# Performance work log

Measured on AMD Instinct MI355X. Metric: run time of the kernel, lower is better.

The kernel has to match this reference:

```python
import jax, jax.numpy as jnp
import numpy as np

L, D_MODEL, D_INNER, DT_RANK, D_STATE, D_CONV, VOCAB = 4, 768, 1536, 48, 16, 4, 32000
B, S = 1, 1024


def rmsnorm(x, w, eps=1e-5):
    return x * jax.lax.rsqrt(jnp.mean(x * x, axis=-1, keepdims=True) + eps) * w


def causal_depthwise_conv(x, w, b):
    # x: [B,S,D]; w: [D,1,K] (torch Conv1d groups=D weight layout); causal left-pad K-1
    y = jax.lax.conv_general_dilated(
        x.transpose(0, 2, 1), w, window_strides=(1,), padding=[(D_CONV - 1, 0)],
        dimension_numbers=('NCH', 'OIH', 'NCH'), feature_group_count=D_INNER)
    return y.transpose(0, 2, 1) + b


def selective_scan(u, dt, A, Bm, Cm, Dv):
    # Faithful to the source: A_delta = exp(dt (x) A), clamp(min=-20) is a no-op on exp output
    A_delta = jnp.clip(jnp.exp(jnp.einsum('bld,dn->bldn', dt, A)), -20.0, None)
    B_delta_u = jnp.einsum('bld,bld,bln->bldn', dt, u, Bm)
    shifted = jnp.pad(A_delta[:, 1:], ((0, 0), (1, 0), (0, 0), (0, 0)))
    A_cum = jnp.exp(jnp.cumsum(shifted, axis=1))
    h = B_delta_u / (A_cum + 1e-12)
    y = jnp.einsum('bldn,bln->bld', jnp.cumsum(h, axis=1) * A_cum, Cm)
    return y + u * Dv


def setup_inputs() -> dict:
    key = jax.random.key(0)
    ks = jax.random.split(key, 8)
    return {
        'tokens': jax.random.randint(ks[0], (B, S), 0, VOCAB),
        'embedding': jax.random.normal(ks[1], (VOCAB, D_MODEL), jnp.float32) * 0.02,
        'norm_w': jnp.ones((L, D_MODEL), jnp.float32),
        'in_proj_w': jax.random.normal(ks[2], (L, 2 * D_INNER, D_MODEL), jnp.float32) * 0.02,
        'conv_w': jax.random.normal(ks[3], (L, D_INNER, 1, D_CONV), jnp.float32) * 0.2,
        'conv_b': jnp.zeros((L, D_INNER), jnp.float32),
        'x_proj_w': jax.random.normal(ks[4], (L, DT_RANK + 2 * D_STATE, D_INNER), jnp.float32) * 0.02,
        'dt_proj_w': jax.random.normal(ks[5], (L, D_INNER, DT_RANK), jnp.float32) * 0.001,
        'dt_proj_b': jnp.full((L, D_INNER), 5.0, jnp.float32),  # delta~5 keeps exp(cumsum(exp(dt*A))) finite
        'A_log': jnp.tile(jnp.log(jnp.arange(1, D_STATE + 1, dtype=jnp.float32)), (L, D_INNER, 1)),
        'D_skip': jnp.ones((L, D_INNER), jnp.float32),
        'out_proj_w': jax.random.normal(ks[6], (L, D_MODEL, D_INNER), jnp.float32) * 0.02,
        'final_norm_w': jnp.ones((D_MODEL,), jnp.float32),
    }


def reference(tokens, embedding, norm_w, in_proj_w, conv_w, conv_b, x_proj_w,
              dt_proj_w, dt_proj_b, A_log, D_skip, out_proj_w, final_norm_w):
    x = embedding[tokens]  # [B,S,d_model]
    for i in range(L):
        h = rmsnorm(x, norm_w[i])
        xz = h @ in_proj_w[i].T                      # [B,S,2*d_inner]
        xi, res = xz[..., :D_INNER], xz[..., D_INNER:]
        xi = jax.nn.silu(causal_depthwise_conv(xi, conv_w[i], conv_b[i]))
        proj = xi @ x_proj_w[i].T                    # [B,S,dt_rank+2*d_state]
        dt = jax.nn.softplus(proj[..., :DT_RANK] @ dt_proj_w[i].T + dt_proj_b[i])
        Bm = proj[..., DT_RANK:DT_RANK + D_STATE]
        Cm = proj[..., DT_RANK + D_STATE:]
        A = -jnp.exp(A_log[i])                       # [d_inner, d_state]
        y = selective_scan(xi, dt, A, Bm, Cm, D_skip[i])
        x = x + (y * jax.nn.silu(res)) @ out_proj_w[i].T
    return rmsnorm(x, final_norm_w) @ embedding.T    # tied LM head: [B,S,vocab]
```

## Files before the change

### kernel.cpp

```cpp
#include <hip/hip_runtime.h>
#include <hip/hip_bf16.h>
#include <cmath>

namespace {

constexpr int kL      = 4;
constexpr int kDModel = 768;
constexpr int kDInner = 1536;
constexpr int kDtRank = 48;
constexpr int kDState = 16;
constexpr int kDConv  = 4;
constexpr int kSeq    = 1024;
constexpr int kPLd    = 96;
constexpr int kPB     = 128;
constexpr int kVocab  = 32000;
constexpr int kCH     = 64;
constexpr int kNCH    = kSeq / kCH;
constexpr int kDN     = kDInner * kDState;

using short8 = __attribute__((ext_vector_type(8))) short;
using f32x4  = __attribute__((ext_vector_type(4))) float;

__device__ __forceinline__ float silu_f(float v) {
    return v / (1.f + __expf(-v));
}

__device__ __forceinline__ void split_bf16(float v, __hip_bfloat16& hi, __hip_bfloat16& lo) {
    hi = __float2bfloat16(v);
    lo = __float2bfloat16(v - __bfloat162float(hi));
}

__global__ void __launch_bounds__(256) f2b_kernel(
    const float* __restrict__ src, __hip_bfloat16* __restrict__ dst, int n) {
    int i = (blockIdx.x * 256 + threadIdx.x) * 4;
    const int stride = gridDim.x * 256 * 4;
    for (; i + 3 < n; i += stride) {
        const float4 v = *reinterpret_cast<const float4*>(src + i);
        dst[i + 0] = __float2bfloat16(v.x);
        dst[i + 1] = __float2bfloat16(v.y);
        dst[i + 2] = __float2bfloat16(v.z);
        dst[i + 3] = __float2bfloat16(v.w);
    }
}

__global__ void __launch_bounds__(256) split3_kernel(
    const float* __restrict__ src, int ldsrc, int rows, int cols,
    __hip_bfloat16* __restrict__ dst, int rowsPad) {
    const int idx = blockIdx.x * 256 + threadIdx.x;
    if (idx >= rowsPad * cols) return;
    const int r = idx / cols, c = idx % cols;
    const float v = (r < rows) ? src[(size_t)r * ldsrc + c] : 0.f;
    __hip_bfloat16 hi, lo;
    split_bf16(v, hi, lo);
    __hip_bfloat16* row = dst + (size_t)r * 3 * cols;
    row[c] = hi; row[cols + c] = hi; row[2 * cols + c] = lo;
}

__global__ void __launch_bounds__(256) dup2_kernel(
    const float* __restrict__ src, __hip_bfloat16* __restrict__ dst, int rows, int cols) {
    const int idx = blockIdx.x * 256 + threadIdx.x;
    if (idx >= rows * cols) return;
    const int r = idx / cols, c = idx % cols;
    const __hip_bfloat16 hi = __float2bfloat16(src[(size_t)r * cols + c]);
    __hip_bfloat16* row = dst + (size_t)r * 2 * cols;
    row[c] = hi; row[cols + c] = hi;
}

__global__ void __launch_bounds__(256) split3x_kernel(
    const float* __restrict__ src, __hip_bfloat16* __restrict__ dst) {
    const int idx = blockIdx.x * 256 + threadIdx.x;
    if (idx >= kL * kPB * kDInner) return;
    const int layer = idx / (kPB * kDInner);
    const int rem   = idx % (kPB * kDInner);
    const int r = rem / kDInner, c = rem % kDInner;
    const float v = (r < kDtRank + 2 * kDState)
        ? src[(size_t)layer * (kDtRank + 2 * kDState) * kDInner + (size_t)r * kDInner + c]
        : 0.f;
    __hip_bfloat16 hi, lo;
    split_bf16(v, hi, lo);
    __hip_bfloat16* row = dst + ((size_t)layer * kPB + r) * 3 * kDInner;
    row[c] = hi; row[kDInner + c] = hi; row[2 * kDInner + c] = lo;
}

__global__ void __launch_bounds__(256) embed_rms_kernel(
    const int* __restrict__ tokens, const float* __restrict__ emb,
    const float* __restrict__ w, float* __restrict__ x,
    __hip_bfloat16* __restrict__ h2) {
    const int s = blockIdx.x;
    const int t = tokens[s];
    const float* src = emb + (size_t)t * kDModel;
    float v[3];
    float ss = 0.f;
    #pragma unroll
    for (int j = 0; j < 3; ++j) {
        const int d = threadIdx.x + j * 256;
        v[j] = src[d];
        x[(size_t)s * kDModel + d] = v[j];
        ss = fmaf(v[j], v[j], ss);
    }
    #pragma unroll
    for (int m = 32; m; m >>= 1) ss += __shfl_xor(ss, m);
    __shared__ float red[4];
    if ((threadIdx.x & 63) == 0) red[threadIdx.x >> 6] = ss;
    __syncthreads();
    const float total = red[0] + red[1] + red[2] + red[3];
    const float scale = rsqrtf(total / (float)kDModel + 1e-5f);
    __hip_bfloat16* dst = h2 + (size_t)s * 3 * kDModel;
    #pragma unroll
    for (int j = 0; j < 3; ++j) {
        const int d = threadIdx.x + j * 256;
        const float hv = v[j] * scale * w[d];
        __hip_bfloat16 hi, lo;
        split_bf16(hv, hi, lo);
        dst[d] = hi; dst[kDModel + d] = lo; dst[2 * kDModel + d] = hi;
    }
}

template <bool FINAL>
__global__ void __launch_bounds__(256) reduce_rms_kernel(
    const float* __restrict__ parts, size_t stride,
    const float* __restrict__ w, float* __restrict__ x,
    __hip_bfloat16* __restrict__ out) {
    const int s = blockIdx.x;
    float v[3];
    float ss = 0.f;
    #pragma unroll
    for (int j = 0; j < 3; ++j) {
        const int d = threadIdx.x + j * 256;
        const size_t off = (size_t)s * kDModel + d;
        float acc = x[off];
        #pragma unroll
        for (int p = 0; p < 6; ++p) acc += parts[(size_t)p * stride + off];
        v[j] = acc;
        x[off] = acc;
        ss = fmaf(acc, acc, ss);
    }
    #pragma unroll
    for (int m = 32; m; m >>= 1) ss += __shfl_xor(ss, m);
    __shared__ float red[4];
    if ((threadIdx.x & 63) == 0) red[threadIdx.x >> 6] = ss;
    __syncthreads();
    const float total = red[0] + red[1] + red[2] + red[3];
    const float scale = rsqrtf(total / (float)kDModel + 1e-5f);
    #pragma unroll
    for (int j = 0; j < 3; ++j) {
        const int d = threadIdx.x + j * 256;
        const float hv = v[j] * scale * w[d];
        if (FINAL) {
            out[(size_t)s * kDModel + d] = __float2bfloat16(hv);
        } else {
            __hip_bfloat16 hi, lo;
            split_bf16(hv, hi, lo);
            __hip_bfloat16* dst = out + (size_t)s * 3 * kDModel;
            dst[d] = hi; dst[kDModel + d] = lo; dst[2 * kDModel + d] = hi;
        }
    }
}

template <int BM, int BN, int KSPLIT>
__global__ void __launch_bounds__(256) mfma_gemm(
    const __hip_bfloat16* __restrict__ A, int lda,
    const __hip_bfloat16* __restrict__ B, int ldb,
    float* __restrict__ C, int ldc,
    int N, int K, size_t partStride) {
    constexpr int BK = 32;
    static_assert(BM == 128 && BN == 128, "staging assumes 128x128");
    __shared__ unsigned short As[2][BM * BK];
    __shared__ unsigned short Bs[2][BN * BK];
    const int tid  = threadIdx.x;
    const int lane = tid & 63;

    const int nwg = gridDim.x * gridDim.y;
    int bid = blockIdx.y * gridDim.x + blockIdx.x;
    {
        const int q = nwg >> 3, r = nwg & 7;
        const int xcd = bid & 7, pos = bid >> 3;
        bid = (xcd < r ? xcd * (q + 1) : r * (q + 1) + (xcd - r) * q) + pos;
    }
    const int m0 = (bid % gridDim.x) * BM;
    const int n0 = (bid / gridDim.x) * BN;

    const int Kp = K / KSPLIT;
    const int kbeg = (KSPLIT > 1) ? blockIdx.z * Kp : 0;
    float* Cw = (KSPLIT > 1) ? C + (size_t)blockIdx.z * partStride : C;
    constexpr int WM = BM / 2, WN = BN / 2;
    constexpr int MR = WM / 16, NR = WN / 16;
    const int wave = tid >> 6;
    const int wm = (wave >> 1) * WM, wn = (wave & 1) * WN;
    const int l15 = lane & 15, l4 = lane >> 4;
    f32x4 acc[MR][NR] = {};

    auto stage = [&](int buf, int k0) {
        #pragma unroll
        for (int i = 0; i < 2; ++i) {
            const int idx = tid + i * 256;
            const int r = idx >> 2, qv = idx & 3;
            const int qs = qv ^ ((r >> 1) & 3);
            __builtin_amdgcn_global_load_lds(
                (const __attribute__((address_space(1))) void*)(A + (size_t)(m0 + r) * lda + k0 + qs * 8),
                (__attribute__((address_space(3))) void*)(&As[buf][(idx - lane) * 8]),
                16, 0, 0);
        }
        #pragma unroll
        for (int i = 0; i < 2; ++i) {
            const int idx = tid + i * 256;
            const int r = idx >> 2, qv = idx & 3;
            const int qs = qv ^ ((r >> 1) & 3);
            __builtin_amdgcn_global_load_lds(
                (const __attribute__((address_space(1))) void*)(B + (size_t)(n0 + r) * ldb + k0 + qs * 8),
                (__attribute__((address_space(3))) void*)(&Bs[buf][(idx - lane) * 8]),
                16, 0, 0);
        }
    };

    const int nt = Kp / BK;
    int cur = 0;
    stage(0, kbeg);
    for (int t = 0; t < nt; ++t) {
        if (t + 1 < nt) {
            stage(cur ^ 1, kbeg + (t + 1) * BK);
            asm volatile("s_waitcnt vmcnt(4)" ::: "memory");
        } else {
            asm volatile("s_waitcnt vmcnt(0)" ::: "memory");
        }
        __builtin_amdgcn_s_barrier();

        short8 af[MR], bfv[NR];
        #pragma unroll
        for (int mi = 0; mi < MR; ++mi) {
            const int R = wm + mi * 16 + l15;
            af[mi] = *reinterpret_cast<const short8*>(&As[cur][(R * 4 + (l4 ^ ((R >> 1) & 3))) * 8]);
        }
        #pragma unroll
        for (int ni = 0; ni < NR; ++ni) {
            const int R = wn + ni * 16 + l15;
            bfv[ni] = *reinterpret_cast<const short8*>(&Bs[cur][(R * 4 + (l4 ^ ((R >> 1) & 3))) * 8]);
        }
        #pragma unroll
        for (int mi = 0; mi < MR; ++mi)
            #pragma unroll
            for (int ni = 0; ni < NR; ++ni)
                acc[mi][ni] = __builtin_amdgcn_mfma_f32_16x16x32_bf16(
                    af[mi], bfv[ni], acc[mi][ni], 0, 0, 0);

        asm volatile("s_waitcnt lgkmcnt(0)" ::: "memory");
        __builtin_amdgcn_s_barrier();
        cur ^= 1;
    }

    #pragma unroll
    for (int mi = 0; mi < MR; ++mi) {
        const int mrow = m0 + wm + mi * 16 + l4 * 4;
        #pragma unroll
        for (int ni = 0; ni < NR; ++ni) {
            const int ncol = n0 + wn + ni * 16 + l15;
            if (ncol >= N) continue;
            #pragma unroll
            for (int r = 0; r < 4; ++r)
                Cw[(size_t)(mrow + r) * ldc + ncol] = acc[mi][ni][r];
        }
    }
}

template <int NP>
__global__ void __launch_bounds__(256) reduce_parts(
    const float* __restrict__ parts, size_t stride,
    float* __restrict__ dst, int count) {
    const int i = (blockIdx.x * 256 + threadIdx.x) * 4;
    if (i >= count) return;
    float4 s = *reinterpret_cast<const float4*>(parts + i);
    #pragma unroll
    for (int p = 1; p < NP; ++p) {
        const float4 v = *reinterpret_cast<const float4*>(parts + (size_t)p * stride + i);
        s.x += v.x; s.y += v.y; s.z += v.z; s.w += v.w;
    }
    *reinterpret_cast<float4*>(dst + i) = s;
}

__global__ void __launch_bounds__(256) conv_silu_kernel(
    const float* __restrict__ p0, const float* __restrict__ p1,
    const float* __restrict__ cw, const float* __restrict__ cb,
    float* __restrict__ xi, __hip_bfloat16* __restrict__ xi2) {
    const int s = blockIdx.x;
    const int d = blockIdx.y * 256 + threadIdx.x;
    float acc = cb[d];
    #pragma unroll
    for (int k = 0; k < kDConv; ++k) {
        const int sl = s - (kDConv - 1) + k;
        if (sl >= 0) {
            const size_t off = (size_t)sl * (2 * kDInner) + d;
            acc = fmaf(p0[off] + p1[off], cw[d * kDConv + k], acc);
        }
    }
    const float v = silu_f(acc);
    xi[(size_t)s * kDInner + d] = v;
    __hip_bfloat16 hi, lo;
    split_bf16(v, hi, lo);
    __hip_bfloat16* row = xi2 + (size_t)s * 3 * kDInner;
    row[d] = hi; row[kDInner + d] = lo; row[2 * kDInner + d] = hi;
}


__device__ __forceinline__ void compute_dt_tile(
    const float* __restrict__ proj, const float* __restrict__ dtw,
    const float* __restrict__ dtb, int l0, int d0, int tid,
    float (*sP)[kDtRank], float (*sdtw)[kDtRank + 1], float (*sdt)[16]) {
    for (int idx = tid; idx < kCH * kDtRank; idx += 256) {
        const int r = idx / kDtRank, c = idx % kDtRank;
        sP[r][c] = proj[(size_t)(l0 + r) * kPLd + c];
    }
    for (int idx = tid; idx < 16 * kDtRank; idx += 256) {
        const int dd = idx / kDtRank, c = idx % kDtRank;
        sdtw[dd][c] = dtw[(size_t)(d0 + dd) * kDtRank + c];
    }
    __syncthreads();
    #pragma unroll
    for (int e = 0; e < 4; ++e) {
        const int idx = tid + e * 256;
        const int r = idx >> 4, dd = idx & 15;
        float acc = dtb[d0 + dd];
        #pragma unroll
        for (int k = 0; k < kDtRank; ++k)
            acc = fmaf(sP[r][k], sdtw[dd][k], acc);
        acc = (acc > 20.f) ? acc : log1pf(__expf(acc));
        sdt[r][dd] = acc;
    }
}

__global__ void __launch_bounds__(256) scan_part1(
    const float* __restrict__ u, const float* __restrict__ proj,
    const float* __restrict__ A_log, const float* __restrict__ dtw,
    const float* __restrict__ dtb,
    float* __restrict__ P, float* __restrict__ S) {
    __shared__ float sP[kCH][kDtRank];
    __shared__ float sdtw[16][kDtRank + 1];
    __shared__ float sdt[kCH][16], su[kCH][16], sB[kCH][16];
    const int tid = threadIdx.x;
    const int n = tid & 15, dl = tid >> 4;
    const int d0 = blockIdx.x * 16;
    const int l0 = blockIdx.y * kCH;
    for (int idx = tid; idx < kCH * 16; idx += 256) {
        const int r = idx >> 4, c = idx & 15;
        su[r][c] = u[(size_t)(l0 + r) * kDInner + d0 + c];
        sB[r][c] = proj[(size_t)(l0 + r) * kPLd + kDtRank + c];
    }
    compute_dt_tile(proj, dtw, dtb, l0, d0, tid, sP, sdtw, sdt);
    __syncthreads();
    const int d = d0 + dl;
    const float Adn = -__expf(A_log[d * kDState + n]);
    float state = 0.f, sumA = 0.f;
    #pragma unroll 8
    for (int l = 0; l < kCH; ++l) {
        const float dtv = sdt[l][dl];
        const float adelta = __expf(dtv * Adn);
        const float mult = __expf(adelta);
        state = fmaf(state, mult, dtv * su[l][dl] * sB[l][n]);
        sumA += adelta;
    }
    const int dn = d * kDState + n;
    P[(size_t)blockIdx.y * kDN + dn] = __expf(sumA);
    S[(size_t)blockIdx.y * kDN + dn] = state;
}

__global__ void __launch_bounds__(256) scan_part2(
    const float* __restrict__ u, const float* __restrict__ proj,
    const float* __restrict__ A_log, const float* __restrict__ dtw,
    const float* __restrict__ dtb, const float* __restrict__ D_skip,
    const float* __restrict__ P, const float* __restrict__ S,
    const float* __restrict__ res0, const float* __restrict__ res1,
    __hip_bfloat16* __restrict__ g2) {
    __shared__ float sP[kCH][kDtRank];
    __shared__ float sdtw[16][kDtRank + 1];
    __shared__ float sdt[kCH][16], su[kCH][16], sB[kCH][16], sC[kCH][16];
    __shared__ float sy[kCH][16];
    const int tid = threadIdx.x;
    const int n = tid & 15, dl = tid >> 4;
    const int d0 = blockIdx.x * 16;
    const int l0 = blockIdx.y * kCH;
    for (int idx = tid; idx < kCH * 16; idx += 256) {
        const int r = idx >> 4, c = idx & 15;
        su[r][c] = u[(size_t)(l0 + r) * kDInner + d0 + c];
        sB[r][c] = proj[(size_t)(l0 + r) * kPLd + kDtRank + c];
        sC[r][c] = proj[(size_t)(l0 + r) * kPLd + kDtRank + kDState + c];
    }
    compute_dt_tile(proj, dtw, dtb, l0, d0, tid, sP, sdtw, sdt);
    const int dn = d0 * kDState + tid;
    float state = 0.f;
    for (int jj = 0; jj < (int)blockIdx.y; ++jj) {
        const size_t idx = (size_t)jj * kDN + dn;
        state = fmaf(state, P[idx], S[idx]);
    }
    __syncthreads();
    const int d = d0 + dl;
    const float Adn = -__expf(A_log[d * kDState + n]);
    const float Dv  = D_skip[d];
    for (int l = 0; l < kCH; ++l) {
        const float dtv = sdt[l][dl];
        const float uv  = su[l][dl];
        const float mult = __expf(__expf(dtv * Adn));
        state = fmaf(state, mult, dtv * uv * sB[l][n]);
        float contrib = state * sC[l][n];
        contrib += __shfl_xor(contrib, 8);
        contrib += __shfl_xor(contrib, 4);
        contrib += __shfl_xor(contrib, 2);
        contrib += __shfl_xor(contrib, 1);
        if (n == 0) sy[l][dl] = fmaf(uv, Dv, contrib);
    }
    __syncthreads();
    for (int idx = tid; idx < kCH * 16; idx += 256) {
        const int r = idx >> 4, c = idx & 15;
        const size_t roff = (size_t)(l0 + r) * (2 * kDInner) + kDInner + d0 + c;
        const float res = res0[roff] + res1[roff];
        const float v = sy[r][c] * silu_f(res);
        __hip_bfloat16 hi, lo;
        split_bf16(v, hi, lo);
        __hip_bfloat16* row = g2 + (size_t)(l0 + r) * 2 * kDInner;
        row[d0 + c] = hi; row[kDInner + d0 + c] = lo;
    }
}

}

extern "C" void kernel_launch(void* const* d_in, const int* in_sizes, int n_in,
                              void* d_out, int out_size, void* d_ws, size_t ws_size,
                              hipStream_t stream) {
    const int*   tokens       = (const int*)d_in[0];
    const float* embedding    = (const float*)d_in[1];
    const float* norm_w       = (const float*)d_in[2];
    const float* in_proj_w    = (const float*)d_in[3];
    const float* conv_w       = (const float*)d_in[4];
    const float* conv_b       = (const float*)d_in[5];
    const float* x_proj_w     = (const float*)d_in[6];
    const float* dt_proj_w    = (const float*)d_in[7];
    const float* dt_proj_b    = (const float*)d_in[8];
    const float* A_log        = (const float*)d_in[9];
    const float* D_skip       = (const float*)d_in[10];
    const float* out_proj_w   = (const float*)d_in[11];
    const float* final_norm_w = (const float*)d_in[12];
    float* out = (float*)d_out;

    constexpr int K3m = 3 * kDModel;
    constexpr int K3i = 3 * kDInner;
    constexpr int K2i = 2 * kDInner;

    char* ws = (char*)d_ws;
    auto alloc = [&](size_t bytes) { char* p = ws; ws += (bytes + 255) & ~(size_t)255; return p; };
    float* x    = (float*)alloc((size_t)kSeq * kDModel * 4);
    float* xi   = (float*)alloc((size_t)kSeq * kDInner * 4);
    float* proj = (float*)alloc((size_t)kSeq * kPLd * 4);
    float* scanP  = (float*)alloc((size_t)kNCH * kDN * 4);
    float* scanS  = (float*)alloc((size_t)kNCH * kDN * 4);
    float* partsXZ = (float*)alloc((size_t)2 * kSeq * 2 * kDInner * 4);
    float* partsP  = (float*)alloc((size_t)24 * kSeq * kPLd * 4);
    float* partsO  = (float*)alloc((size_t)6 * kSeq * kDModel * 4);
    __hip_bfloat16* h_bf   = (__hip_bfloat16*)alloc((size_t)kSeq * kDModel * 2);
    __hip_bfloat16* h2     = (__hip_bfloat16*)alloc((size_t)kSeq * K3m * 2);
    __hip_bfloat16* xi2    = (__hip_bfloat16*)alloc((size_t)kSeq * K3i * 2);
    __hip_bfloat16* g2     = (__hip_bfloat16*)alloc((size_t)kSeq * K2i * 2);
    __hip_bfloat16* emb_bf = (__hip_bfloat16*)alloc((size_t)kVocab * kDModel * 2);
    __hip_bfloat16* inw2   = (__hip_bfloat16*)alloc((size_t)kL * 2 * kDInner * K3m * 2);
    __hip_bfloat16* outw2  = (__hip_bfloat16*)alloc((size_t)kL * kDModel * K2i * 2);
    __hip_bfloat16* xw2    = (__hip_bfloat16*)alloc((size_t)kL * kPB * K3i * 2);

    f2b_kernel<<<4096, 256, 0, stream>>>(embedding, emb_bf, kVocab * kDModel);
    dup2_kernel<<<(kL * kDModel * kDInner + 255) / 256, 256, 0, stream>>>(
        out_proj_w, outw2, kL * kDModel, kDInner);
    split3_kernel<<<(kL * 2 * kDInner * kDModel + 255) / 256, 256, 0, stream>>>(
        in_proj_w, kDModel, kL * 2 * kDInner, kDModel, inw2, kL * 2 * kDInner);
    split3x_kernel<<<(kL * kPB * kDInner + 255) / 256, 256, 0, stream>>>(
        x_proj_w, xw2);

    embed_rms_kernel<<<kSeq, 256, 0, stream>>>(tokens, embedding, norm_w, x, h2);

    for (int i = 0; i < kL; ++i) {
        mfma_gemm<128, 128, 2><<<dim3(kSeq / 128, 2 * kDInner / 128, 2), 256, 0, stream>>>(
            h2, K3m, inw2 + (size_t)i * 2 * kDInner * K3m, K3m,
            partsXZ, 2 * kDInner, 2 * kDInner, K3m, (size_t)kSeq * 2 * kDInner);

        conv_silu_kernel<<<dim3(kSeq, kDInner / 256), 256, 0, stream>>>(
            partsXZ, partsXZ + (size_t)kSeq * 2 * kDInner,
            conv_w + (size_t)i * kDInner * kDConv, conv_b + (size_t)i * kDInner,
            xi, xi2);

        mfma_gemm<128, 128, 24><<<dim3(kSeq / 128, 1, 24), 256, 0, stream>>>(
            xi2, K3i, xw2 + (size_t)i * kPB * K3i, K3i,
            partsP, kPLd, kPLd, K3i, (size_t)kSeq * kPLd);
        reduce_parts<24><<<(kSeq * kPLd / 4 + 255) / 256, 256, 0, stream>>>(
            partsP, (size_t)kSeq * kPLd, proj, kSeq * kPLd);

        const float* A_l  = A_log + (size_t)i * kDInner * kDState;
        const float* dtw  = dt_proj_w + (size_t)i * kDInner * kDtRank;
        const float* dtb  = dt_proj_b + (size_t)i * kDInner;
        scan_part1<<<dim3(kDInner / 16, kNCH), 256, 0, stream>>>(
            xi, proj, A_l, dtw, dtb, scanP, scanS);
        scan_part2<<<dim3(kDInner / 16, kNCH), 256, 0, stream>>>(
            xi, proj, A_l, dtw, dtb, D_skip + (size_t)i * kDInner,
            scanP, scanS, partsXZ, partsXZ + (size_t)kSeq * 2 * kDInner, g2);

        mfma_gemm<128, 128, 6><<<dim3(kSeq / 128, kDModel / 128, 6), 256, 0, stream>>>(
            g2, K2i, outw2 + (size_t)i * kDModel * K2i, K2i,
            partsO, kDModel, kDModel, K2i, (size_t)kSeq * kDModel);

        if (i + 1 < kL) {
            reduce_rms_kernel<false><<<kSeq, 256, 0, stream>>>(
                partsO, (size_t)kSeq * kDModel, norm_w + (size_t)(i + 1) * kDModel, x, h2);
        } else {
            reduce_rms_kernel<true><<<kSeq, 256, 0, stream>>>(
                partsO, (size_t)kSeq * kDModel, final_norm_w, x, h_bf);
        }
    }

    mfma_gemm<128, 128, 1><<<dim3(kSeq / 128, kVocab / 128, 1), 256, 0, stream>>>(
        h_bf, kDModel, emb_bf, kDModel, out, kVocab, kVocab, kDModel, 0);
}
```

Baseline: 777.6 us.

## Vectorize weight conversion kernels and raise split-K factors for in/out projections

The f32-to-bf16 weight conversion and duplication kernels now process four or eight elements per thread with vector loads and packed stores, instead of scalar element-wise writes. Split-K for the in_proj GEMM rises from 2 to 4 and for out_proj from 6 to 8, giving more blocks per launch. The consumers (conv_silu, scan_part2, reduce_rms) now sum a variable number of partial buffers. In exchange, the larger split writes and reads more fp32 partial data per layer.

```diff
diff --git a/kernel.cpp b/kernel.cpp
--- a/kernel.cpp
+++ b/kernel.cpp
@@ -17,12 +17,19 @@
 constexpr int kCH     = 64;
 constexpr int kNCH    = kSeq / kCH;
 constexpr int kDN     = kDInner * kDState;
+constexpr int kSplitIn  = 4;
+constexpr int kSplitOut = 8;
 
 using short8 = __attribute__((ext_vector_type(8))) short;
 using f32x4  = __attribute__((ext_vector_type(4))) float;
 
 __device__ __forceinline__ float silu_f(float v) {
     return v / (1.f + __expf(-v));
+}
+
+__device__ __forceinline__ unsigned short f2bu(float v) {
+    __hip_bfloat16 h = __float2bfloat16(v);
+    return *reinterpret_cast<unsigned short*>(&h);
 }
 
 __device__ __forceinline__ void split_bf16(float v, __hip_bfloat16& hi, __hip_bfloat16& lo) {
@@ -30,56 +37,78 @@
     lo = __float2bfloat16(v - __bfloat162float(hi));
 }
 
+__device__ __forceinline__ void split_u(float v, unsigned short& hi, unsigned short& lo) {
+    __hip_bfloat16 h, l;
+    split_bf16(v, h, l);
+    hi = *reinterpret_cast<unsigned short*>(&h);
+    lo = *reinterpret_cast<unsigned short*>(&l);
+}
+
 __global__ void __launch_bounds__(256) f2b_kernel(
     const float* __restrict__ src, __hip_bfloat16* __restrict__ dst, int n) {
-    int i = (blockIdx.x * 256 + threadIdx.x) * 4;
-    const int stride = gridDim.x * 256 * 4;
-    for (; i + 3 < n; i += stride) {
-        const float4 v = *reinterpret_cast<const float4*>(src + i);
-        dst[i + 0] = __float2bfloat16(v.x);
-        dst[i + 1] = __float2bfloat16(v.y);
-        dst[i + 2] = __float2bfloat16(v.z);
-        dst[i + 3] = __float2bfloat16(v.w);
+    int i = (blockIdx.x * 256 + threadIdx.x) * 8;
+    const int stride = gridDim.x * 256 * 8;
+    for (; i + 7 < n; i += stride) {
+        const float4 a = *reinterpret_cast<const float4*>(src + i);
+        const float4 b = *reinterpret_cast<const float4*>(src + i + 4);
+        union { unsigned short u[8]; uint4 v; } pk;
+        pk.u[0] = f2bu(a.x); pk.u[1] = f2bu(a.y); pk.u[2] = f2bu(a.z); pk.u[3] = f2bu(a.w);
+        pk.u[4] = f2bu(b.x); pk.u[5] = f2bu(b.y); pk.u[6] = f2bu(b.z); pk.u[7] = f2bu(b.w);
+        *reinterpret_cast<uint4*>(reinterpret_cast<unsigned short*>(dst) + i) = pk.v;
     }
 }
 
 __global__ void __launch_bounds__(256) split3_kernel(
-    const float* __restrict__ src, int ldsrc, int rows, int cols,
-    __hip_bfloat16* __restrict__ dst, int rowsPad) {
+    const float* __restrict__ src, int rows, int cols,
+    __hip_bfloat16* __restrict__ dst) {
     const int idx = blockIdx.x * 256 + threadIdx.x;
-    if (idx >= rowsPad * cols) return;
-    const int r = idx / cols, c = idx % cols;
-    const float v = (r < rows) ? src[(size_t)r * ldsrc + c] : 0.f;
-    __hip_bfloat16 hi, lo;
-    split_bf16(v, hi, lo);
-    __hip_bfloat16* row = dst + (size_t)r * 3 * cols;
-    row[c] = hi; row[cols + c] = hi; row[2 * cols + c] = lo;
+    const int c4cnt = cols >> 2;
+    if (idx >= rows * c4cnt) return;
+    const int r = idx / c4cnt, c = (idx % c4cnt) << 2;
+    const float4 v = *reinterpret_cast<const float4*>(src + (size_t)r * cols + c);
+    ushort4 hi4, lo4;
+    split_u(v.x, hi4.x, lo4.x); split_u(v.y, hi4.y, lo4.y);
+    split_u(v.z, hi4.z, lo4.z); split_u(v.w, hi4.w, lo4.w);
+    unsigned short* row = reinterpret_cast<unsigned short*>(dst) + (size_t)r * 3 * cols;
+    *reinterpret_cast<ushort4*>(row + c) = hi4;
+    *reinterpret_cast<ushort4*>(row + cols + c) = hi4;
+    *reinterpret_cast<ushort4*>(row + 2 * cols + c) = lo4;
 }
 
 __global__ void __launch_bounds__(256) dup2_kernel(
-    const float* __restrict__ src, __hip_bfloat16* __restrict__ dst, int rows, int cols) {
+    const float* __restrict__ src, __hip_bfloat16* __restrict__ dst,
+    int rows, int cols) {
     const int idx = blockIdx.x * 256 + threadIdx.x;
-    if (idx >= rows * cols) return;
-    const int r = idx / cols, c = idx % cols;
-    const __hip_bfloat16 hi = __float2bfloat16(src[(size_t)r * cols + c]);
-    __hip_bfloat16* row = dst + (size_t)r * 2 * cols;
-    row[c] = hi; row[cols + c] = hi;
+    const int c4cnt = cols >> 2;
+    if (idx >= rows * c4cnt) return;
+    const int r = idx / c4cnt, c = (idx % c4cnt) << 2;
+    const float4 v = *reinterpret_cast<const float4*>(src + (size_t)r * cols + c);
+    ushort4 hi4 = {f2bu(v.x), f2bu(v.y), f2bu(v.z), f2bu(v.w)};
+    unsigned short* row = reinterpret_cast<unsigned short*>(dst) + (size_t)r * 2 * cols;
+    *reinterpret_cast<ushort4*>(row + c) = hi4;
+    *reinterpret_cast<ushort4*>(row + cols + c) = hi4;
 }
 
 __global__ void __launch_bounds__(256) split3x_kernel(
     const float* __restrict__ src, __hip_bfloat16* __restrict__ dst) {
     const int idx = blockIdx.x * 256 + threadIdx.x;
-    if (idx >= kL * kPB * kDInner) return;
-    const int layer = idx / (kPB * kDInner);
-    const int rem   = idx % (kPB * kDInner);
-    const int r = rem / kDInner, c = rem % kDInner;
-    const float v = (r < kDtRank + 2 * kDState)
-        ? src[(size_t)layer * (kDtRank + 2 * kDState) * kDInner + (size_t)r * kDInner + c]
-        : 0.f;
-    __hip_bfloat16 hi, lo;
-    split_bf16(v, hi, lo);
-    __hip_bfloat16* row = dst + ((size_t)layer * kPB + r) * 3 * kDInner;
-    row[c] = hi; row[kDInner + c] = hi; row[2 * kDInner + c] = lo;
+    constexpr int c4cnt = kDInner >> 2;
+    if (idx >= kL * kPB * c4cnt) return;
+    const int layer = idx / (kPB * c4cnt);
+    const int rem   = idx % (kPB * c4cnt);
+    const int r = rem / c4cnt, c = (rem % c4cnt) << 2;
+    float4 v = {0.f, 0.f, 0.f, 0.f};
+    if (r < kDtRank + 2 * kDState)
+        v = *reinterpret_cast<const float4*>(
+            src + (size_t)layer * (kDtRank + 2 * kDState) * kDInner + (size_t)r * kDInner + c);
+    ushort4 hi4, lo4;
+    split_u(v.x, hi4.x, lo4.x); split_u(v.y, hi4.y, lo4.y);
+    split_u(v.z, hi4.z, lo4.z); split_u(v.w, hi4.w, lo4.w);
+    unsigned short* row = reinterpret_cast<unsigned short*>(dst)
+        + ((size_t)layer * kPB + r) * 3 * kDInner;
+    *reinterpret_cast<ushort4*>(row + c) = hi4;
+    *reinterpret_cast<ushort4*>(row + kDInner + c) = hi4;
+    *reinterpret_cast<ushort4*>(row + 2 * kDInner + c) = lo4;
 }
 
 __global__ void __launch_bounds__(256) embed_rms_kernel(
@@ -130,7 +159,7 @@
         const size_t off = (size_t)s * kDModel + d;
         float acc = x[off];
         #pragma unroll
-        for (int p = 0; p < 6; ++p) acc += parts[(size_t)p * stride + off];
+        for (int p = 0; p < kSplitOut; ++p) acc += parts[(size_t)p * stride + off];
         v[j] = acc;
         x[off] = acc;
         ss = fmaf(acc, acc, ss);
@@ -278,7 +307,7 @@
 }
 
 __global__ void __launch_bounds__(256) conv_silu_kernel(
-    const float* __restrict__ p0, const float* __restrict__ p1,
+    const float* __restrict__ parts, size_t stride,
     const float* __restrict__ cw, const float* __restrict__ cb,
     float* __restrict__ xi, __hip_bfloat16* __restrict__ xi2) {
     const int s = blockIdx.x;
@@ -289,7 +318,10 @@
         const int sl = s - (kDConv - 1) + k;
         if (sl >= 0) {
             const size_t off = (size_t)sl * (2 * kDInner) + d;
-            acc = fmaf(p0[off] + p1[off], cw[d * kDConv + k], acc);
+            float xzv = parts[off];
+            #pragma unroll
+            for (int p = 1; p < kSplitIn; ++p) xzv += parts[(size_t)p * stride + off];
+            acc = fmaf(xzv, cw[d * kDConv + k], acc);
         }
     }
     const float v = silu_f(acc);
@@ -367,7 +399,7 @@
     const float* __restrict__ A_log, const float* __restrict__ dtw,
     const float* __restrict__ dtb, const float* __restrict__ D_skip,
     const float* __restrict__ P, const float* __restrict__ S,
-    const float* __restrict__ res0, const float* __restrict__ res1,
+    const float* __restrict__ resparts, size_t rstride,
     __hip_bfloat16* __restrict__ g2) {
     __shared__ float sP[kCH][kDtRank];
     __shared__ float sdtw[16][kDtRank + 1];
@@ -410,7 +442,9 @@
     for (int idx = tid; idx < kCH * 16; idx += 256) {
         const int r = idx >> 4, c = idx & 15;
         const size_t roff = (size_t)(l0 + r) * (2 * kDInner) + kDInner + d0 + c;
-        const float res = res0[roff] + res1[roff];
+        float res = resparts[roff];
+        #pragma unroll
+        for (int p = 1; p < kSplitIn; ++p) res += resparts[(size_t)p * rstride + roff];
         const float v = sy[r][c] * silu_f(res);
         __hip_bfloat16 hi, lo;
         split_bf16(v, hi, lo);
@@ -450,9 +484,9 @@
     float* proj = (float*)alloc((size_t)kSeq * kPLd * 4);
     float* scanP  = (float*)alloc((size_t)kNCH * kDN * 4);
     float* scanS  = (float*)alloc((size_t)kNCH * kDN * 4);
-    float* partsXZ = (float*)alloc((size_t)2 * kSeq * 2 * kDInner * 4);
+    float* partsXZ = (float*)alloc((size_t)kSplitIn * kSeq * 2 * kDInner * 4);
     float* partsP  = (float*)alloc((size_t)24 * kSeq * kPLd * 4);
-    float* partsO  = (float*)alloc((size_t)6 * kSeq * kDModel * 4);
+    float* partsO  = (float*)alloc((size_t)kSplitOut * kSeq * kDModel * 4);
     __hip_bfloat16* h_bf   = (__hip_bfloat16*)alloc((size_t)kSeq * kDModel * 2);
     __hip_bfloat16* h2     = (__hip_bfloat16*)alloc((size_t)kSeq * K3m * 2);
     __hip_bfloat16* xi2    = (__hip_bfloat16*)alloc((size_t)kSeq * K3i * 2);
@@ -463,22 +497,22 @@
     __hip_bfloat16* xw2    = (__hip_bfloat16*)alloc((size_t)kL * kPB * K3i * 2);
 
     f2b_kernel<<<4096, 256, 0, stream>>>(embedding, emb_bf, kVocab * kDModel);
-    dup2_kernel<<<(kL * kDModel * kDInner + 255) / 256, 256, 0, stream>>>(
+    dup2_kernel<<<(kL * kDModel * kDInner / 4 + 255) / 256, 256, 0, stream>>>(
         out_proj_w, outw2, kL * kDModel, kDInner);
-    split3_kernel<<<(kL * 2 * kDInner * kDModel + 255) / 256, 256, 0, stream>>>(
-        in_proj_w, kDModel, kL * 2 * kDInner, kDModel, inw2, kL * 2 * kDInner);
-    split3x_kernel<<<(kL * kPB * kDInner + 255) / 256, 256, 0, stream>>>(
+    split3_kernel<<<(kL * 2 * kDInner * kDModel / 4 + 255) / 256, 256, 0, stream>>>(
+        in_proj_w, kL * 2 * kDInner, kDModel, inw2);
+    split3x_kernel<<<(kL * kPB * kDInner / 4 + 255) / 256, 256, 0, stream>>>(
         x_proj_w, xw2);
 
     embed_rms_kernel<<<kSeq, 256, 0, stream>>>(tokens, embedding, norm_w, x, h2);
 
     for (int i = 0; i < kL; ++i) {
-        mfma_gemm<128, 128, 2><<<dim3(kSeq / 128, 2 * kDInner / 128, 2), 256, 0, stream>>>(
+        mfma_gemm<128, 128, kSplitIn><<<dim3(kSeq / 128, 2 * kDInner / 128, kSplitIn), 256, 0, stream>>>(
             h2, K3m, inw2 + (size_t)i * 2 * kDInner * K3m, K3m,
             partsXZ, 2 * kDInner, 2 * kDInner, K3m, (size_t)kSeq * 2 * kDInner);
 
         conv_silu_kernel<<<dim3(kSeq, kDInner / 256), 256, 0, stream>>>(
-            partsXZ, partsXZ + (size_t)kSeq * 2 * kDInner,
+            partsXZ, (size_t)kSeq * 2 * kDInner,
             conv_w + (size_t)i * kDInner * kDConv, conv_b + (size_t)i * kDInner,
             xi, xi2);
 
@@ -495,9 +529,9 @@
             xi, proj, A_l, dtw, dtb, scanP, scanS);
         scan_part2<<<dim3(kDInner / 16, kNCH), 256, 0, stream>>>(
             xi, proj, A_l, dtw, dtb, D_skip + (size_t)i * kDInner,
-            scanP, scanS, partsXZ, partsXZ + (size_t)kSeq * 2 * kDInner, g2);
-
-        mfma_gemm<128, 128, 6><<<dim3(kSeq / 128, kDModel / 128, 6), 256, 0, stream>>>(
+            scanP, scanS, partsXZ, (size_t)kSeq * 2 * kDInner, g2);
+
+        mfma_gemm<128, 128, kSplitOut><<<dim3(kSeq / 128, kDModel / 128, kSplitOut), 256, 0, stream>>>(
             g2, K2i, outw2 + (size_t)i * kDModel * K2i, K2i,
             partsO, kDModel, kDModel, K2i, (size_t)kSeq * kDModel);
 
```

Result: no change. 767.6 us (-1.3%).
